# Performance work log

Hardware: AMD Instinct MI355X
Metric: run time of the kernel (lower is better)

## Reference

```python
import jax, jax.numpy as jnp
from jax import lax
import numpy as np

B, N_MEL, T_MEL = 256, 80, 800
R = 16                      # n_frames_per_step
RNN = 1024                  # decoder_rnn_dim
ENC = 256                   # token_embedding_size
MEL_DIM = N_MEL * R         # 1280, == RNN + ENC (LSTMCell input size)
IN_DIM = RNN + ENC          # 1280


def setup_inputs() -> dict:
    key = jax.random.key(0)
    ks = jax.random.split(key, 10)
    s = 0.02
    return {
        "context": jax.random.normal(ks[0], (B, ENC), dtype=jnp.float32),
        "target": jax.random.normal(ks[1], (B, N_MEL, T_MEL), dtype=jnp.float32),
        "W_ih": jax.random.normal(ks[2], (4 * RNN, IN_DIM), dtype=jnp.float32) * s,
        "b_ih": jnp.zeros((4 * RNN,), dtype=jnp.float32),
        "W_hh": jax.random.normal(ks[3], (4 * RNN, RNN), dtype=jnp.float32) * s,
        "b_hh": jnp.zeros((4 * RNN,), dtype=jnp.float32),
        "W_proj": jax.random.normal(ks[4], (MEL_DIM, IN_DIM), dtype=jnp.float32) * s,
        "b_proj": jnp.zeros((MEL_DIM,), dtype=jnp.float32),
        "W_gate": jax.random.normal(ks[5], (1, IN_DIM), dtype=jnp.float32) * s,
        "b_gate": jnp.zeros((1,), dtype=jnp.float32),
    }


def _decoder_forward(context, target, W_ih, b_ih, W_hh, b_hh, W_proj, b_proj, W_gate, b_gate):
    b = context.shape[0]
    n_mel, t_mel = target.shape[1], target.shape[2]
    mel_dim = W_proj.shape[0]
    r = mel_dim // n_mel                      # n_frames_per_step
    T = t_mel // r                            # decoder steps
    rnn = W_hh.shape[1]

    # parse_decoder_inputs: [B, n_mel, T_mel] -> [T, B, mel_dim]
    frames = target.transpose(0, 2, 1).reshape(b, T, mel_dim).transpose(1, 0, 2)
    # step 0 uses the all-zeros go frame; step t>=1 uses target frame t (teacher forcing, p=1)
    inputs = frames.at[0].set(0.0)

    h0 = jnp.zeros((b, rnn), dtype=context.dtype)
    c0 = jnp.zeros((b, rnn), dtype=context.dtype)

    def step(carry, x):
        h, c = carry
        gates = x @ W_ih.T + b_ih + h @ W_hh.T + b_hh   # [B, 4*rnn]
        i, f, g, o = jnp.split(gates, 4, axis=-1)        # torch LSTMCell gate order
        c_new = jax.nn.sigmoid(f) * c + jax.nn.sigmoid(i) * jnp.tanh(g)
        h_new = jax.nn.sigmoid(o) * jnp.tanh(c_new)
        # eval mode: dropout on c is identity
        oc = jnp.concatenate([h_new, context], axis=1)   # [B, rnn+enc]
        mel = oc @ W_proj.T + b_proj                     # [B, mel_dim]
        gate = oc @ W_gate.T + b_gate                    # [B, 1]
        return (h_new, c_new), (mel, gate)

    _, (mels, gates) = lax.scan(step, (h0, c0), inputs)
    # mels: [T, B, mel_dim] -> [B, n_mel, T_mel]
    mel_outputs = mels.transpose(1, 0, 2).reshape(b, T * r, n_mel).transpose(0, 2, 1)
    gate_outputs = gates.transpose(1, 0, 2)              # [B, T, 1]
    return mel_outputs, gate_outputs


def reference(context, target, W_ih, b_ih, W_hh, b_hh, W_proj, b_proj, W_gate, b_gate):
    return _decoder_forward(context, target, W_ih, b_ih, W_hh, b_hh,
                            W_proj, b_proj, W_gate, b_gate)
```

## Files before the change

kernel.cpp:

```cpp
#include <hip/hip_runtime.h>
#include <hip/hip_bf16.h>
#include <math.h>

#define BB     256
#define NMEL   80
#define TMEL   800
#define NFR    16
#define TT     50
#define RNN    1024
#define ENC    256
#define INDIM  1280
#define G4     4096
#define MROWS  (TT*BB)

typedef __attribute__((ext_vector_type(8))) short bf16x8;
typedef __attribute__((ext_vector_type(4))) float f32x4;

#define GAS __attribute__((address_space(1)))
#define LAS __attribute__((address_space(3)))

__device__ __forceinline__ unsigned short f2bf(float f) {
    unsigned int u = __float_as_uint(f);
    u += 0x7FFFu + ((u >> 16) & 1u);
    return (unsigned short)(u >> 16);
}
__device__ __forceinline__ float bf2f(unsigned short s) {
    return __uint_as_float(((unsigned int)s) << 16);
}
__device__ __forceinline__ float fsig(float x) {
    return 1.f / (1.f + __expf(-x));
}
__device__ __forceinline__ float ftanh(float x) {
    return 2.f / (1.f + __expf(-2.f * x)) - 1.f;
}


__global__ void k_f32_to_bf16(const float* __restrict__ src,
                              unsigned short* __restrict__ dst, int n4) {
    for (int i = blockIdx.x * blockDim.x + threadIdx.x; i < n4;
         i += gridDim.x * blockDim.x) {
        f32x4 v = *(const f32x4*)(src + (size_t)i * 4);
        unsigned long long p = (unsigned long long)f2bf(v[0]) |
                               ((unsigned long long)f2bf(v[1]) << 16) |
                               ((unsigned long long)f2bf(v[2]) << 32) |
                               ((unsigned long long)f2bf(v[3]) << 48);
        *(unsigned long long*)(dst + (size_t)i * 4) = p;
    }
}

__global__ void k_conv_wph(const float* __restrict__ wproj,
                           unsigned short* __restrict__ dst) {
    const int n4 = INDIM * RNN / 4;
    for (int i = blockIdx.x * blockDim.x + threadIdx.x; i < n4;
         i += gridDim.x * blockDim.x) {
        int mp = i >> 8, kc = (i & 255) * 4;
        int mel = mp >> 4, fr = mp & 15;
        f32x4 v = *(const f32x4*)(wproj + (size_t)(fr * NMEL + mel) * INDIM + kc);
        unsigned long long p = (unsigned long long)f2bf(v[0]) |
                               ((unsigned long long)f2bf(v[1]) << 16) |
                               ((unsigned long long)f2bf(v[2]) << 32) |
                               ((unsigned long long)f2bf(v[3]) << 48);
        *(unsigned long long*)(dst + (size_t)i * 4) = p;
    }
}

__global__ __launch_bounds__(128) void k_frames(const float* __restrict__ target,
                                                unsigned short* __restrict__ frames) {
    const int wg = blockIdx.x;
    const int t = wg >> 8, b = wg & 255;
    unsigned short* dst = frames + ((size_t)t * BB + b) * INDIM;
    if (t == 0) {
        for (int i = threadIdx.x; i < INDIM / 8; i += 128)
            *(f32x4*)(dst + i * 8) = (f32x4){0.f, 0.f, 0.f, 0.f};
        return;
    }
    __shared__ float ld[NMEL][17];
    for (int i = threadIdx.x; i < 320; i += 128) {
        const int mel = i >> 2, fq = i & 3;
        f32x4 v = *(const f32x4*)(target + ((size_t)b * NMEL + mel) * TMEL +
                                  t * NFR + fq * 4);
        #pragma unroll
        for (int j = 0; j < 4; ++j) ld[mel][fq * 4 + j] = v[j];
    }
    __syncthreads();
    for (int i = threadIdx.x; i < 160; i += 128) {
        unsigned long long p0 = 0, p1 = 0;
        #pragma unroll
        for (int j = 0; j < 4; ++j) {
            const int k = i * 8 + j;
            p0 |= (unsigned long long)f2bf(ld[k % 80][k / 80]) << (16 * j);
        }
        #pragma unroll
        for (int j = 0; j < 4; ++j) {
            const int k = i * 8 + 4 + j;
            p1 |= (unsigned long long)f2bf(ld[k % 80][k / 80]) << (16 * j);
        }
        *(unsigned long long*)(dst + i * 8) = p0;
        *(unsigned long long*)(dst + i * 8 + 4) = p1;
    }
}

__global__ void k_ctxproj(const float* __restrict__ context,
                          const float* __restrict__ wproj,
                          const float* __restrict__ bproj,
                          float* __restrict__ ctx) {
    int i = blockIdx.x * blockDim.x + threadIdx.x;
    if (i >= BB * INDIM) return;
    int mp = i % INDIM, b = i / INDIM;
    int mel = mp >> 4, fr = mp & 15;
    int m = fr * NMEL + mel;
    const float* wr = wproj + (size_t)m * INDIM + RNN;
    const float* cb = context + b * ENC;
    float acc = bproj[m];
    for (int e = 0; e < ENC; ++e) acc += cb[e] * wr[e];
    ctx[(size_t)b * INDIM + mp] = acc;
}

__global__ void k_gatectx(const float* __restrict__ context,
                          const float* __restrict__ wgate,
                          const float* __restrict__ bgate,
                          float* __restrict__ gctx) {
    int b = blockIdx.x * blockDim.x + threadIdx.x;
    if (b >= BB) return;
    float acc = bgate[0];
    const float* cb = context + b * ENC;
    for (int e = 0; e < ENC; ++e) acc += cb[e] * wgate[RNN + e];
    gctx[b] = acc;
}

template<int STRIDE, int KDIM>
__device__ __forceinline__ void gemm_core2(const unsigned short* __restrict__ A,
                                           const unsigned short* __restrict__ Bw,
                                           int mblk, int nblk,
                                           unsigned short* As,
                                           unsigned short* Bs,
                                           f32x4 acc[4][2]) {
    const int tid = threadIdx.x, lane = tid & 63, w = tid >> 6;
    const int lr = lane & 15, q = lane >> 4;
    const int wm = (w >> 2) * 64, wn = (w & 3) * 32;
    const int cc1 = tid, cc2 = tid + 512;
    const int r1 = cc1 >> 3, s1 = ((cc1 & 7) ^ (r1 & 7)) * 8;
    const int r2 = cc2 >> 3, s2 = ((cc2 & 7) ^ (r2 & 7)) * 8;
    const unsigned short* a1p = A + (size_t)(mblk + r1) * STRIDE + s1;
    const unsigned short* a2p = A + (size_t)(mblk + r2) * STRIDE + s2;
    const unsigned short* b1p = Bw + (size_t)(nblk + r1) * STRIDE + s1;
    const unsigned short* b2p = Bw + (size_t)(nblk + r2) * STRIDE + s2;

#define GSTAGE(buf, k0) do {                                                   \
    __builtin_amdgcn_global_load_lds((const GAS unsigned int*)(a1p + (k0)),    \
        (LAS unsigned int*)(As + (buf) * 8192 + w * 512), 16, 0, 0);           \
    __builtin_amdgcn_global_load_lds((const GAS unsigned int*)(a2p + (k0)),    \
        (LAS unsigned int*)(As + (buf) * 8192 + 4096 + w * 512), 16, 0, 0);    \
    __builtin_amdgcn_global_load_lds((const GAS unsigned int*)(b1p + (k0)),    \
        (LAS unsigned int*)(Bs + (buf) * 8192 + w * 512), 16, 0, 0);           \
    __builtin_amdgcn_global_load_lds((const GAS unsigned int*)(b2p + (k0)),    \
        (LAS unsigned int*)(Bs + (buf) * 8192 + 4096 + w * 512), 16, 0, 0); } while (0)

    constexpr int NIT = KDIM / 64;
    GSTAGE(0, 0);
    #pragma unroll 4
    for (int it = 0; it < NIT; ++it) {
        if (it < NIT - 1) {
            GSTAGE((it + 1) & 1, (it + 1) * 64);
            asm volatile("s_waitcnt vmcnt(4)" ::: "memory");
        } else {
            asm volatile("s_waitcnt vmcnt(0)" ::: "memory");
        }
        asm volatile("s_barrier" ::: "memory");
        __builtin_amdgcn_sched_barrier(0);
        const unsigned short* Ab = As + (it & 1) * 8192;
        const unsigned short* Bb = Bs + (it & 1) * 8192;
        #pragma unroll
        for (int ks = 0; ks < 2; ++ks) {
            const int j = (((ks * 4 + q) ^ (lr & 7)) * 8);
            bf16x8 af[4], bv[2];
            #pragma unroll
            for (int mi = 0; mi < 4; ++mi)
                af[mi] = *(const bf16x8*)(Ab + (wm + mi * 16 + lr) * 64 + j);
            #pragma unroll
            for (int ni = 0; ni < 2; ++ni)
                bv[ni] = *(const bf16x8*)(Bb + (wn + ni * 16 + lr) * 64 + j);
            #pragma unroll
            for (int mi = 0; mi < 4; ++mi)
                #pragma unroll
                for (int ni = 0; ni < 2; ++ni)
                    acc[mi][ni] = __builtin_amdgcn_mfma_f32_16x16x32_bf16(
                        af[mi], bv[ni], acc[mi][ni], 0, 0, 0);
        }
        asm volatile("s_waitcnt lgkmcnt(0)" ::: "memory");
        __builtin_amdgcn_sched_barrier(0);
        asm volatile("s_barrier" ::: "memory");
    }
#undef GSTAGE
}

__global__ __launch_bounds__(512) void k_gemm_xproj(
    const unsigned short* __restrict__ A,
    const unsigned short* __restrict__ Bw,
    const float* __restrict__ b_ih, const float* __restrict__ b_hh,
    unsigned short* __restrict__ Cout)
{
    __shared__ unsigned short As[2][8192], Bs[2][8192];
    f32x4 acc[4][2] = {};
    const int mblk = blockIdx.y * 128, nblk = blockIdx.x * 128;
    gemm_core2<INDIM, INDIM>(A, Bw, mblk, nblk, &As[0][0], &Bs[0][0], acc);
    const int lane = threadIdx.x & 63, w = threadIdx.x >> 6;
    const int wm = (w >> 2) * 64, wn = (w & 3) * 32;
    const int lr = lane & 15, q = lane >> 4;
    #pragma unroll
    for (int ni = 0; ni < 2; ++ni) {
        const int col = nblk + wn + ni * 16 + lr;
        const float bias = b_ih[col] + b_hh[col];
        #pragma unroll
        for (int mi = 0; mi < 4; ++mi) {
            const int row0 = mblk + wm + mi * 16 + q * 4;
            #pragma unroll
            for (int r = 0; r < 4; ++r)
                Cout[(size_t)(row0 + r) * G4 + col] = f2bf(acc[mi][ni][r] + bias);
        }
    }
}

__global__ __launch_bounds__(512) void k_gemm_mel(
    const unsigned short* __restrict__ A,
    const unsigned short* __restrict__ Bw,
    const float* __restrict__ ctxproj,
    float* __restrict__ out0)
{
    __shared__ unsigned short As[2][8192], Bs[2][8192];
    __shared__ float txp[8][16][20];
    f32x4 acc[4][2] = {};
    const int mblk = blockIdx.y * 128, nblk = blockIdx.x * 128;
    gemm_core2<RNN, RNN>(A, Bw, mblk, nblk, &As[0][0], &Bs[0][0], acc);
    const int lane = threadIdx.x & 63, w = threadIdx.x >> 6;
    const int wm = (w >> 2) * 64, wn = (w & 3) * 32;
    const int lr = lane & 15, q = lane >> 4;
    const int rbase = q * 4;
    const int rowl = lane & 15, fq = lane >> 4;
    #pragma unroll
    for (int mi = 0; mi < 4; ++mi) {
        const int row0 = mblk + wm + mi * 16;
        const int t = row0 >> 8, b0 = row0 & 255;
        #pragma unroll
        for (int ni = 0; ni < 2; ++ni) {
            const int colbase = nblk + wn + ni * 16;
            const int mel = colbase >> 4;
            #pragma unroll
            for (int r = 0; r < 4; ++r)
                txp[w][rbase + r][lr] = acc[mi][ni][r];
            const int bL = b0 + rowl;
            f32x4 v = *(const f32x4*)&txp[w][rowl][fq * 4];
            f32x4 cx = *(const f32x4*)(ctxproj + (size_t)bL * INDIM +
                                       mel * 16 + fq * 4);
            *(f32x4*)(out0 + (size_t)(bL * NMEL + mel) * TMEL +
                      t * NFR + fq * 4) = v + cx;
        }
    }
}

__global__ __launch_bounds__(512) void k_step(
    const unsigned short* __restrict__ Whh,
    const unsigned short* __restrict__ xproj_t,
    const unsigned short* __restrict__ h_prev,
    unsigned short* __restrict__ h_next,
    float* __restrict__ c)
{
    __shared__ unsigned short Abuf[3][8192];
    __shared__ unsigned short Bbuf[3][8192];
    __shared__ unsigned short xg[4096];
    __shared__ float cld[64][16];
    __shared__ float gates[4][64][17];
    const int tid = threadIdx.x, lane = tid & 63, w = tid >> 6;
    const int g = w & 3, mh = w >> 2;
    const int n0 = blockIdx.x * 16, m0 = blockIdx.y * 64;
    const int lr = lane & 15, q = lane >> 4;

    const int cc1 = tid, cc2 = tid + 512;
    const int r1 = cc1 >> 4, s1g = (cc1 & 15) ^ (r1 & 15);
    const int r2 = cc2 >> 4, s2g = (cc2 & 15) ^ (r2 & 15);
    const unsigned short* a1src = h_prev + (size_t)(m0 + r1) * RNN + s1g * 8;
    const unsigned short* a2src = h_prev + (size_t)(m0 + r2) * RNN + s2g * 8;
    const unsigned short* b1src = Whh +
        (size_t)((r1 >> 4) * RNN + n0 + (r1 & 15)) * RNN + s1g * 8;
    const unsigned short* b2src = Whh +
        (size_t)((r2 >> 4) * RNN + n0 + (r2 & 15)) * RNN + s2g * 8;
    const unsigned short* xsrc = xproj_t +
        (size_t)(m0 + ((tid >> 1) & 63)) * G4 + (tid >> 7) * RNN + n0 +
        (tid & 1) * 8;
    const float* csrc = c + (size_t)(m0 + (tid >> 2)) * RNN + n0 + (tid & 3) * 4;

#define STAGE(buf, k0) do {                                                    \
    __builtin_amdgcn_global_load_lds((const GAS unsigned int*)(a1src + (k0)),  \
        (LAS unsigned int*)&Abuf[buf][w * 512], 16, 0, 0);                     \
    __builtin_amdgcn_global_load_lds((const GAS unsigned int*)(a2src + (k0)),  \
        (LAS unsigned int*)&Abuf[buf][4096 + w * 512], 16, 0, 0);              \
    __builtin_amdgcn_global_load_lds((const GAS unsigned int*)(b1src + (k0)),  \
        (LAS unsigned int*)&Bbuf[buf][w * 512], 16, 0, 0);                     \
    __builtin_amdgcn_global_load_lds((const GAS unsigned int*)(b2src + (k0)),  \
        (LAS unsigned int*)&Bbuf[buf][4096 + w * 512], 16, 0, 0); } while (0)

    if (w < 4)
        __builtin_amdgcn_global_load_lds((const GAS unsigned int*)csrc,
            (LAS unsigned int*)&cld[w * 16][0], 16, 0, 0);
    __builtin_amdgcn_global_load_lds((const GAS unsigned int*)xsrc,
        (LAS unsigned int*)&xg[w * 512], 16, 0, 0);
    STAGE(0, 0); STAGE(1, 128);

    f32x4 acc[2] = {};
    #pragma unroll
    for (int it = 0; it < 8; ++it) {
        if (it <= 6) asm volatile("s_waitcnt vmcnt(4)" ::: "memory");
        else         asm volatile("s_waitcnt vmcnt(0)" ::: "memory");
        asm volatile("s_waitcnt lgkmcnt(0)" ::: "memory");
        asm volatile("s_barrier" ::: "memory");
        __builtin_amdgcn_sched_barrier(0);
        if (it <= 5) STAGE((it + 2) % 3, (it + 2) * 128);
        const unsigned short* Ab = Abuf[it % 3];
        const unsigned short* Bb = Bbuf[it % 3];
        #pragma unroll
        for (int ks = 0; ks < 4; ++ks) {
            const int j = ((ks * 4 + q) ^ lr) * 8;
            bf16x8 a0 = *(const bf16x8*)(Ab + (mh * 32 + lr) * 128 + j);
            bf16x8 a1 = *(const bf16x8*)(Ab + (mh * 32 + 16 + lr) * 128 + j);
            bf16x8 bv = *(const bf16x8*)(Bb + (g * 16 + lr) * 128 + j);
            acc[0] = __builtin_amdgcn_mfma_f32_16x16x32_bf16(a0, bv, acc[0], 0, 0, 0);
            acc[1] = __builtin_amdgcn_mfma_f32_16x16x32_bf16(a1, bv, acc[1], 0, 0, 0);
        }
    }

    #pragma unroll
    for (int mi = 0; mi < 2; ++mi)
        #pragma unroll
        for (int r = 0; r < 4; ++r) {
            const int row = mh * 32 + mi * 16 + q * 4 + r;
            gates[g][row][lr] = acc[mi][r] +
                bf2f(xg[(g * 64 + row) * 16 + lr]);
        }
    __syncthreads();

    #pragma unroll
    for (int q2 = 0; q2 < 2; ++q2) {
        const int e = tid + q2 * 512;
        const int row = e >> 4, col = e & 15;
        const int b = m0 + row, j = n0 + col;
        const float xi = gates[0][row][col];
        const float xf = gates[1][row][col];
        const float xgt = gates[2][row][col];
        const float xo = gates[3][row][col];
        const float si = fsig(xi);
        const float sf = fsig(xf);
        const float so = fsig(xo);
        const float cp = cld[row][col];
        const float cn = sf * cp + si * ftanh(xgt);
        const float hn = so * ftanh(cn);
        c[(size_t)b * RNN + j] = cn;
        h_next[(size_t)b * RNN + j] = f2bf(hn);
    }
#undef STAGE
}

__global__ void k_gate(const unsigned short* __restrict__ h,
                       const float* __restrict__ wgate,
                       const float* __restrict__ gctx,
                       float* __restrict__ out1) {
    const int gw = (blockIdx.x * blockDim.x + threadIdx.x) >> 6;
    const int lane = threadIdx.x & 63;
    if (gw >= MROWS) return;
    const unsigned short* hr = h + (size_t)gw * RNN + lane * 16;
    const float* wr = wgate + lane * 16;
    float acc = 0.f;
    #pragma unroll
    for (int j = 0; j < 16; ++j) acc += bf2f(hr[j]) * wr[j];
    for (int off = 32; off; off >>= 1) acc += __shfl_down(acc, off);
    if (lane == 0) {
        const int t = gw >> 8, b = gw & 255;
        out1[b * TT + t] = acc + gctx[b];
    }
}

static const size_t OFF_WIH   = 0;
static const size_t OFF_WHH   = OFF_WIH   + (size_t)G4 * INDIM * 2;
static const size_t OFF_WPH   = OFF_WHH   + (size_t)G4 * RNN * 2;
static const size_t OFF_FRM   = OFF_WPH   + (size_t)INDIM * RNN * 2;
static const size_t OFF_XPROJ = OFF_FRM   + (size_t)MROWS * INDIM * 2;
static const size_t OFF_HALL  = OFF_XPROJ + (size_t)MROWS * G4 * 2;
static const size_t OFF_C     = OFF_HALL  + (size_t)(TT + 1) * BB * RNN * 2;
static const size_t OFF_CTX   = OFF_C     + (size_t)BB * RNN * 4;
static const size_t OFF_GCTX  = OFF_CTX   + (size_t)BB * INDIM * 4;

extern "C" void kernel_launch(void* const* d_in, const int* in_sizes, int n_in,
                              void* d_out, int out_size, void* d_ws, size_t ws_size,
                              hipStream_t stream) {
    const float* context = (const float*)d_in[0];
    const float* target  = (const float*)d_in[1];
    const float* W_ih    = (const float*)d_in[2];
    const float* b_ih    = (const float*)d_in[3];
    const float* W_hh    = (const float*)d_in[4];
    const float* b_hh    = (const float*)d_in[5];
    const float* W_proj  = (const float*)d_in[6];
    const float* b_proj  = (const float*)d_in[7];
    const float* W_gate  = (const float*)d_in[8];
    const float* b_gate  = (const float*)d_in[9];
    float* out = (float*)d_out;
    char* ws = (char*)d_ws;

    unsigned short* wih_bf  = (unsigned short*)(ws + OFF_WIH);
    unsigned short* whh_bf  = (unsigned short*)(ws + OFF_WHH);
    unsigned short* wph_bf  = (unsigned short*)(ws + OFF_WPH);
    unsigned short* frames  = (unsigned short*)(ws + OFF_FRM);
    unsigned short* xproj   = (unsigned short*)(ws + OFF_XPROJ);
    unsigned short* h_all   = (unsigned short*)(ws + OFF_HALL);
    float*          c_buf   = (float*)(ws + OFF_C);
    float*          ctxproj = (float*)(ws + OFF_CTX);
    float*          gctx    = (float*)(ws + OFF_GCTX);

    hipMemsetAsync(h_all, 0, (size_t)BB * RNN * 2, stream);
    hipMemsetAsync(c_buf, 0, (size_t)BB * RNN * 4, stream);

    k_f32_to_bf16<<<2048, 256, 0, stream>>>(W_ih, wih_bf, G4 * INDIM / 4);
    k_f32_to_bf16<<<2048, 256, 0, stream>>>(W_hh, whh_bf, G4 * RNN / 4);
    k_conv_wph<<<2048, 256, 0, stream>>>(W_proj, wph_bf);
    k_frames<<<MROWS, 128, 0, stream>>>(target, frames);
    k_ctxproj<<<(BB * INDIM + 255) / 256, 256, 0, stream>>>(context, W_proj,
                                                            b_proj, ctxproj);
    k_gatectx<<<1, 256, 0, stream>>>(context, W_gate, b_gate, gctx);

    k_gemm_xproj<<<dim3(G4 / 128, MROWS / 128), 512, 0, stream>>>(
        frames, wih_bf, b_ih, b_hh, xproj);

    for (int t = 0; t < TT; ++t) {
        k_step<<<dim3(64, 4), 512, 0, stream>>>(
            whh_bf, xproj + (size_t)t * BB * G4,
            h_all + (size_t)t * BB * RNN,
            h_all + (size_t)(t + 1) * BB * RNN, c_buf);
    }

    k_gemm_mel<<<dim3(INDIM / 128, MROWS / 128), 512, 0, stream>>>(
        h_all + (size_t)BB * RNN, wph_bf, ctxproj, out);
    k_gate<<<MROWS / 4, 256, 0, stream>>>(h_all + (size_t)BB * RNN, W_gate,
                                          gctx, out + (size_t)BB * NMEL * TMEL);
}
```

Before: 753.8 us.

## Triple-buffer GEMM LDS staging and move context projection to MFMA GEMM

The shared GEMM core now keeps three LDS stages instead of two, prefetching two tiles ahead with one barrier per iteration instead of two. This is meant to hide global-load latency in the xproj and mel GEMMs. The scalar fp32 context-projection kernel is replaced by a bf16 conversion of context and the projection weights plus an MFMA GEMM, which lowers the precision of that term. The extra LDS raises per-block shared memory use, which may reduce occupancy.

```diff
diff --git a/kernel.cpp b/kernel.cpp
--- a/kernel.cpp
+++ b/kernel.cpp
@@ -64,6 +64,23 @@
     }
 }
 
+__global__ void k_conv_wpc(const float* __restrict__ wproj,
+                           unsigned short* __restrict__ dst) {
+    const int n4 = INDIM * ENC / 4;
+    for (int i = blockIdx.x * blockDim.x + threadIdx.x; i < n4;
+         i += gridDim.x * blockDim.x) {
+        int mp = i >> 6, kc = (i & 63) * 4;
+        int mel = mp >> 4, fr = mp & 15;
+        f32x4 v = *(const f32x4*)(wproj + (size_t)(fr * NMEL + mel) * INDIM +
+                                  RNN + kc);
+        unsigned long long p = (unsigned long long)f2bf(v[0]) |
+                               ((unsigned long long)f2bf(v[1]) << 16) |
+                               ((unsigned long long)f2bf(v[2]) << 32) |
+                               ((unsigned long long)f2bf(v[3]) << 48);
+        *(unsigned long long*)(dst + (size_t)i * 4) = p;
+    }
+}
+
 __global__ __launch_bounds__(128) void k_frames(const float* __restrict__ target,
                                                 unsigned short* __restrict__ frames) {
     const int wg = blockIdx.x;
@@ -98,22 +115,6 @@
         *(unsigned long long*)(dst + i * 8) = p0;
         *(unsigned long long*)(dst + i * 8 + 4) = p1;
     }
-}
-
-__global__ void k_ctxproj(const float* __restrict__ context,
-                          const float* __restrict__ wproj,
-                          const float* __restrict__ bproj,
-                          float* __restrict__ ctx) {
-    int i = blockIdx.x * blockDim.x + threadIdx.x;
-    if (i >= BB * INDIM) return;
-    int mp = i % INDIM, b = i / INDIM;
-    int mel = mp >> 4, fr = mp & 15;
-    int m = fr * NMEL + mel;
-    const float* wr = wproj + (size_t)m * INDIM + RNN;
-    const float* cb = context + b * ENC;
-    float acc = bproj[m];
-    for (int e = 0; e < ENC; ++e) acc += cb[e] * wr[e];
-    ctx[(size_t)b * INDIM + mp] = acc;
 }
 
 __global__ void k_gatectx(const float* __restrict__ context,
@@ -129,7 +130,7 @@
 }
 
 template<int STRIDE, int KDIM>
-__device__ __forceinline__ void gemm_core2(const unsigned short* __restrict__ A,
+__device__ __forceinline__ void gemm_core3(const unsigned short* __restrict__ A,
                                            const unsigned short* __restrict__ Bw,
                                            int mblk, int nblk,
                                            unsigned short* As,
@@ -157,19 +158,17 @@
         (LAS unsigned int*)(Bs + (buf) * 8192 + 4096 + w * 512), 16, 0, 0); } while (0)
 
     constexpr int NIT = KDIM / 64;
-    GSTAGE(0, 0);
-    #pragma unroll 4
+    GSTAGE(0, 0); GSTAGE(1, 64);
+    #pragma unroll 3
     for (int it = 0; it < NIT; ++it) {
-        if (it < NIT - 1) {
-            GSTAGE((it + 1) & 1, (it + 1) * 64);
-            asm volatile("s_waitcnt vmcnt(4)" ::: "memory");
-        } else {
-            asm volatile("s_waitcnt vmcnt(0)" ::: "memory");
-        }
+        if (it < NIT - 1) asm volatile("s_waitcnt vmcnt(4)" ::: "memory");
+        else              asm volatile("s_waitcnt vmcnt(0)" ::: "memory");
+        asm volatile("s_waitcnt lgkmcnt(0)" ::: "memory");
         asm volatile("s_barrier" ::: "memory");
         __builtin_amdgcn_sched_barrier(0);
-        const unsigned short* Ab = As + (it & 1) * 8192;
-        const unsigned short* Bb = Bs + (it & 1) * 8192;
+        if (it <= NIT - 3) GSTAGE((it + 2) % 3, (it + 2) * 64);
+        const unsigned short* Ab = As + (it % 3) * 8192;
+        const unsigned short* Bb = Bs + (it % 3) * 8192;
         #pragma unroll
         for (int ks = 0; ks < 2; ++ks) {
             const int j = (((ks * 4 + q) ^ (lr & 7)) * 8);
@@ -187,9 +186,6 @@
                     acc[mi][ni] = __builtin_amdgcn_mfma_f32_16x16x32_bf16(
                         af[mi], bv[ni], acc[mi][ni], 0, 0, 0);
         }
-        asm volatile("s_waitcnt lgkmcnt(0)" ::: "memory");
-        __builtin_amdgcn_sched_barrier(0);
-        asm volatile("s_barrier" ::: "memory");
     }
 #undef GSTAGE
 }
@@ -200,10 +196,10 @@
     const float* __restrict__ b_ih, const float* __restrict__ b_hh,
     unsigned short* __restrict__ Cout)
 {
-    __shared__ unsigned short As[2][8192], Bs[2][8192];
+    __shared__ unsigned short As[3][8192], Bs[3][8192];
     f32x4 acc[4][2] = {};
     const int mblk = blockIdx.y * 128, nblk = blockIdx.x * 128;
-    gemm_core2<INDIM, INDIM>(A, Bw, mblk, nblk, &As[0][0], &Bs[0][0], acc);
+    gemm_core3<INDIM, INDIM>(A, Bw, mblk, nblk, &As[0][0], &Bs[0][0], acc);
     const int lane = threadIdx.x & 63, w = threadIdx.x >> 6;
     const int wm = (w >> 2) * 64, wn = (w & 3) * 32;
     const int lr = lane & 15, q = lane >> 4;
@@ -227,11 +223,11 @@
     const float* __restrict__ ctxproj,
     float* __restrict__ out0)
 {
-    __shared__ unsigned short As[2][8192], Bs[2][8192];
+    __shared__ unsigned short As[3][8192], Bs[3][8192];
     __shared__ float txp[8][16][20];
     f32x4 acc[4][2] = {};
     const int mblk = blockIdx.y * 128, nblk = blockIdx.x * 128;
-    gemm_core2<RNN, RNN>(A, Bw, mblk, nblk, &As[0][0], &Bs[0][0], acc);
+    gemm_core3<RNN, RNN>(A, Bw, mblk, nblk, &As[0][0], &Bs[0][0], acc);
     const int lane = threadIdx.x & 63, w = threadIdx.x >> 6;
     const int wm = (w >> 2) * 64, wn = (w & 3) * 32;
     const int lr = lane & 15, q = lane >> 4;
@@ -254,6 +250,34 @@
                                        mel * 16 + fq * 4);
             *(f32x4*)(out0 + (size_t)(bL * NMEL + mel) * TMEL +
                       t * NFR + fq * 4) = v + cx;
+        }
+    }
+}
+
+__global__ __launch_bounds__(512) void k_gemm_ctx(
+    const unsigned short* __restrict__ A,
+    const unsigned short* __restrict__ Bw,
+    const float* __restrict__ bproj,
+    float* __restrict__ ctxout)
+{
+    __shared__ unsigned short As[3][8192], Bs[3][8192];
+    f32x4 acc[4][2] = {};
+    const int mblk = blockIdx.y * 128, nblk = blockIdx.x * 128;
+    gemm_core3<ENC, ENC>(A, Bw, mblk, nblk, &As[0][0], &Bs[0][0], acc);
+    const int lane = threadIdx.x & 63, w = threadIdx.x >> 6;
+    const int wm = (w >> 2) * 64, wn = (w & 3) * 32;
+    const int lr = lane & 15, q = lane >> 4;
+    #pragma unroll
+    for (int ni = 0; ni < 2; ++ni) {
+        const int mp = nblk + wn + ni * 16 + lr;
+        const int mel = mp >> 4, fr = mp & 15;
+        const float bias = bproj[fr * NMEL + mel];
+        #pragma unroll
+        for (int mi = 0; mi < 4; ++mi) {
+            const int b0 = mblk + wm + mi * 16 + q * 4;
+            #pragma unroll
+            for (int r = 0; r < 4; ++r)
+                ctxout[(size_t)(b0 + r) * INDIM + mp] = acc[mi][ni][r] + bias;
         }
     }
 }
@@ -381,7 +405,9 @@
 static const size_t OFF_WIH   = 0;
 static const size_t OFF_WHH   = OFF_WIH   + (size_t)G4 * INDIM * 2;
 static const size_t OFF_WPH   = OFF_WHH   + (size_t)G4 * RNN * 2;
-static const size_t OFF_FRM   = OFF_WPH   + (size_t)INDIM * RNN * 2;
+static const size_t OFF_WPC   = OFF_WPH   + (size_t)INDIM * RNN * 2;
+static const size_t OFF_CTXB  = OFF_WPC   + (size_t)INDIM * ENC * 2;
+static const size_t OFF_FRM   = OFF_CTXB  + (size_t)BB * ENC * 2;
 static const size_t OFF_XPROJ = OFF_FRM   + (size_t)MROWS * INDIM * 2;
 static const size_t OFF_HALL  = OFF_XPROJ + (size_t)MROWS * G4 * 2;
 static const size_t OFF_C     = OFF_HALL  + (size_t)(TT + 1) * BB * RNN * 2;
@@ -407,6 +433,8 @@
     unsigned short* wih_bf  = (unsigned short*)(ws + OFF_WIH);
     unsigned short* whh_bf  = (unsigned short*)(ws + OFF_WHH);
     unsigned short* wph_bf  = (unsigned short*)(ws + OFF_WPH);
+    unsigned short* wpc_bf  = (unsigned short*)(ws + OFF_WPC);
+    unsigned short* ctx_bf  = (unsigned short*)(ws + OFF_CTXB);
     unsigned short* frames  = (unsigned short*)(ws + OFF_FRM);
     unsigned short* xproj   = (unsigned short*)(ws + OFF_XPROJ);
     unsigned short* h_all   = (unsigned short*)(ws + OFF_HALL);
@@ -420,10 +448,13 @@
     k_f32_to_bf16<<<2048, 256, 0, stream>>>(W_ih, wih_bf, G4 * INDIM / 4);
     k_f32_to_bf16<<<2048, 256, 0, stream>>>(W_hh, whh_bf, G4 * RNN / 4);
     k_conv_wph<<<2048, 256, 0, stream>>>(W_proj, wph_bf);
+    k_conv_wpc<<<320, 256, 0, stream>>>(W_proj, wpc_bf);
+    k_f32_to_bf16<<<64, 256, 0, stream>>>(context, ctx_bf, BB * ENC / 4);
     k_frames<<<MROWS, 128, 0, stream>>>(target, frames);
-    k_ctxproj<<<(BB * INDIM + 255) / 256, 256, 0, stream>>>(context, W_proj,
-                                                            b_proj, ctxproj);
     k_gatectx<<<1, 256, 0, stream>>>(context, W_gate, b_gate, gctx);
+
+    k_gemm_ctx<<<dim3(INDIM / 128, BB / 128), 512, 0, stream>>>(
+        ctx_bf, wpc_bf, b_proj, ctxproj);
 
     k_gemm_xproj<<<dim3(G4 / 128, MROWS / 128), 512, 0, stream>>>(
         frames, wih_bf, b_ih, b_hh, xproj);
```

Measured after the change: 729.7 us. -3.2%, faster.
